# Performance work log

Measured on AMD Instinct MI355X. Metric: run time of the kernel, lower is better.

## Reference

```python
import jax, jax.numpy as jnp
import numpy as np

C_IN = 256


def setup_inputs() -> dict:
    key = jax.random.key(0)
    ks = jax.random.split(key, 10)
    B, C, H, W = 1, C_IN, 96, 96
    Cq = C // 8
    s = 0.05
    return {
        "x": jax.random.normal(ks[0], (B, C, H, W), dtype=jnp.float32),
        "Wq": jax.random.normal(ks[1], (Cq, C), dtype=jnp.float32) * s,
        "bq": jax.random.normal(ks[2], (Cq,), dtype=jnp.float32) * s,
        "Wk": jax.random.normal(ks[3], (Cq, C), dtype=jnp.float32) * s,
        "bk": jax.random.normal(ks[4], (Cq,), dtype=jnp.float32) * s,
        "Wv": jax.random.normal(ks[5], (C, C), dtype=jnp.float32) * s,
        "bv": jax.random.normal(ks[6], (C,), dtype=jnp.float32) * s,
        "W6": jax.random.normal(ks[7], (C, C), dtype=jnp.float32) * s,
        "b6": jax.random.normal(ks[8], (C,), dtype=jnp.float32) * s,
        "gamma": jnp.ones((1,), dtype=jnp.float32),
    }


def reference(x, Wq, bq, Wk, bk, Wv, bv, W6, b6, gamma):
    # TRM forward (OFS just wraps it). 1x1 convs expressed as einsums.
    B, C, H, W = x.shape
    N = H * W
    scale = C ** -0.5  # 1 / sqrt(in_dim)
    xf = x.reshape(B, C, N)
    q = jnp.einsum('oc,bcn->bon', Wq, xf) + bq[None, :, None]   # (B, C/8, N)
    k = jnp.einsum('oc,bcn->bon', Wk, xf) + bk[None, :, None]   # (B, C/8, N)
    v = jnp.einsum('oc,bcn->bon', Wv, xf) + bv[None, :, None]   # (B, C,   N)
    # energy[b,n,m] = sum_c q[b,c,n] * k[b,c,m]  -> full spatial attention (B,N,N)
    energy = jnp.einsum('bcn,bcm->bnm', q, k)
    att = jax.nn.softmax(energy, axis=-1)
    # out[b,c,n] = sum_m v[b,c,m] * att[b,n,m]
    out = jnp.einsum('bcm,bnm->bcn', v, att)                    # (B, C, N)
    # torch: out.permute(2,0,1) -> (N,B,C); max/mean over C; sum; mean over B
    out_co = out.max(axis=1) + out.mean(axis=1)                 # (B, N)
    x_co = out_co.mean(axis=0).reshape(B, -1) * scale           # valid because B == 1
    x_co = jax.nn.softmax(x_co, axis=-1).reshape(B, 1, H, W)    # spatial gate
    gated = x * x_co
    y = jnp.einsum('oc,bchw->bohw', W6, gated) + b6[None, :, None, None]
    return gamma * y + x + y
```

## Files before the change

### kernel.cpp

```cpp
#include <hip/hip_runtime.h>

#define N 9216
#define CIN 256
#define DQ 32
#define NT 144
#define LOG2E 1.44269504088896340736f

typedef short short8 __attribute__((ext_vector_type(8)));
typedef float floatx4 __attribute__((ext_vector_type(4)));
typedef unsigned short ushort_t;

__device__ __forceinline__ ushort_t f2bf(float f) {
  union { float f; unsigned u; } a; a.f = f;
  unsigned u = a.u;
  u += 0x7fffu + ((u >> 16) & 1u);
  return (ushort_t)(u >> 16);
}
__device__ __forceinline__ ushort_t f2bf_fast(float f) {
  union { float f; unsigned u; } a; a.f = f;
  return (ushort_t)((a.u + 0x8000u) >> 16);
}
__device__ __forceinline__ float bf2f(ushort_t h) {
  union { unsigned u; float f; } a; a.u = ((unsigned)h) << 16;
  return a.f;
}
__device__ __forceinline__ unsigned pack2(float lo, float hi) {
  return ((unsigned)f2bf_fast(hi) << 16) | (unsigned)f2bf_fast(lo);
}
__device__ __forceinline__ short8 mk_bf16x8(const float* p) {
  float4 f0 = *(const float4*)(p);
  float4 f1 = *(const float4*)(p + 4);
  union { unsigned u[4]; short8 v; } r;
  r.u[0] = pack2(f0.x, f0.y);
  r.u[1] = pack2(f0.z, f0.w);
  r.u[2] = pack2(f1.x, f1.y);
  r.u[3] = pack2(f1.z, f1.w);
  return r.v;
}

#define XBT_STRIDE 264

__device__ __forceinline__ void stage_x_tile(
    const float* __restrict__ x, int n0, int t, ushort_t (*xbT)[XBT_STRIDE])
{
  const int p = t & 31, ng = t >> 5;
  unsigned* base = (unsigned*)&xbT[0][0] + (size_t)(ng * 8) * 132;
#pragma unroll
  for (int cc = 0; cc < 4; ++cc) {
    const int c = cc * 64 + 2 * p;
    const float* r0 = x + (size_t)c * N + n0 + ng * 8;
    const float* r1 = r0 + N;
    float4 a0 = *(const float4*)(r0);
    float4 a1 = *(const float4*)(r0 + 4);
    float4 b0 = *(const float4*)(r1);
    float4 b1 = *(const float4*)(r1 + 4);
    unsigned* d = base + (cc * 32 + p);
    d[0 * 132] = pack2(a0.x, b0.x);
    d[1 * 132] = pack2(a0.y, b0.y);
    d[2 * 132] = pack2(a0.z, b0.z);
    d[3 * 132] = pack2(a0.w, b0.w);
    d[4 * 132] = pack2(a1.x, b1.x);
    d[5 * 132] = pack2(a1.y, b1.y);
    d[6 * 132] = pack2(a1.z, b1.z);
    d[7 * 132] = pack2(a1.w, b1.w);
  }
}

__global__ __launch_bounds__(256) void qkv_mfma(
    const float* __restrict__ x,
    const float* __restrict__ Wq, const float* __restrict__ bq,
    const float* __restrict__ Wk, const float* __restrict__ bk,
    const float* __restrict__ Wv, const float* __restrict__ bv,
    ushort_t* __restrict__ qT, ushort_t* __restrict__ kT,
    ushort_t* __restrict__ vG, float* __restrict__ sumExp)
{
  if (blockIdx.x == 0 && blockIdx.y == 0 && threadIdx.x == 0) *sumExp = 0.f;

  __shared__ ushort_t xbT[64][XBT_STRIDE];
  const int t = threadIdx.x;
  const int n0 = blockIdx.x * 64;
  const int oc = blockIdx.y;
  const int w = t >> 6, lane = t & 63;
  const int quad = lane >> 4, l15 = lane & 15;

  stage_x_tile(x, n0, t, xbT);
  __syncthreads();

  const int obase = oc * 64 + w * 16;
  const int oA = obase + l15;
  const float* Arow;
  if (oc == 0) Arow = (obase < 32) ? (Wq + (size_t)oA * CIN)
                                   : (Wk + (size_t)(oA - 32) * CIN);
  else         Arow = Wv + (size_t)(oA - 64) * CIN;

  floatx4 acc[4];
#pragma unroll
  for (int b2 = 0; b2 < 4; ++b2) acc[b2] = (floatx4){0.f, 0.f, 0.f, 0.f};

#pragma unroll
  for (int ks = 0; ks < 8; ++ks) {
    const short8 af = mk_bf16x8(Arow + ks * 32 + 8 * quad);
#pragma unroll
    for (int b2 = 0; b2 < 4; ++b2) {
      const short8 bf = *(const short8*)&xbT[b2 * 16 + l15][ks * 32 + 8 * quad];
      acc[b2] = __builtin_amdgcn_mfma_f32_16x16x32_bf16(af, bf, acc[b2], 0, 0, 0);
    }
  }

#pragma unroll
  for (int b2 = 0; b2 < 4; ++b2) {
    const int n = n0 + b2 * 16 + l15;
#pragma unroll
    for (int r = 0; r < 4; ++r) {
      const int o = obase + 4 * quad + r;
      const float val = acc[b2][r];
      if (oc == 0) {
        if (o < 32) qT[(size_t)n * DQ + o]        = f2bf((val + bq[o]) * LOG2E);
        else        kT[(size_t)n * DQ + (o - 32)] = f2bf(val + bk[o - 32]);
      } else        vG[(size_t)(o - 64) * N + n]  = f2bf(val + bv[o - 64]);
    }
  }
}

__global__ __launch_bounds__(256, 4) void attn_kernel(
    const ushort_t* __restrict__ qT, const ushort_t* __restrict__ kT,
    const ushort_t* __restrict__ vG,
    ushort_t* __restrict__ Opart, float* __restrict__ lpart,
    int base, int rem)
{
  __shared__ ushort_t Pb[2][64][36];

  const int t = threadIdx.x;
  const int w = t >> 6;
  const int lane = t & 63;
  const int quad = lane >> 4;
  const int l15 = lane & 15;
  const int nt = blockIdx.x;
  const int s  = blockIdx.y;
  const int n0 = nt * 64;
  const int sliceIters = base + (s < rem ? 1 : 0);
  const int it0 = s * base + (s < rem ? s : rem);
  const int mbase = it0 * 32;
  const int cw = w * 64;

  short8 aq = *(const short8*)(qT + (size_t)(n0 + 16 * w + l15) * DQ + 8 * quad);

  floatx4 acc[4][4];
#pragma unroll
  for (int a2 = 0; a2 < 4; ++a2)
#pragma unroll
    for (int b2 = 0; b2 < 4; ++b2)
      acc[a2][b2] = (floatx4){0.f, 0.f, 0.f, 0.f};
  float lsum[4] = {0.f, 0.f, 0.f, 0.f};
  const floatx4 z4 = {0.f, 0.f, 0.f, 0.f};

  for (int it = 0; it < sliceIters; ++it) {
    const int m0 = mbase + it * 32;

    short8 kb0 = *(const short8*)(kT + (size_t)(m0 + l15) * DQ + 8 * quad);
    short8 kb1 = *(const short8*)(kT + (size_t)(m0 + 16 + l15) * DQ + 8 * quad);
    floatx4 s0 = __builtin_amdgcn_mfma_f32_16x16x32_bf16(aq, kb0, z4, 0, 0, 0);
    floatx4 s1 = __builtin_amdgcn_mfma_f32_16x16x32_bf16(aq, kb1, z4, 0, 0, 0);

    const ushort_t* vb = vG + (size_t)m0 + 8 * quad;
    short8 av0 = *(const short8*)(vb + (size_t)(cw +  0 + l15) * N);
    short8 av1 = *(const short8*)(vb + (size_t)(cw + 16 + l15) * N);
    short8 av2 = *(const short8*)(vb + (size_t)(cw + 32 + l15) * N);
    short8 av3 = *(const short8*)(vb + (size_t)(cw + 48 + l15) * N);

    ushort_t* pb = &Pb[it & 1][0][0];
#pragma unroll
    for (int r = 0; r < 4; ++r) {
      float p0 = exp2f(s0[r]);
      float p1 = exp2f(s1[r]);
      lsum[r] += p0 + p1;
      const int row = 16 * w + 4 * quad + r;
      pb[row * 36 + l15]      = f2bf_fast(p0);
      pb[row * 36 + 16 + l15] = f2bf_fast(p1);
    }
    __syncthreads();

#pragma unroll
    for (int b2 = 0; b2 < 4; ++b2) {
      const ushort_t* pr = pb + (b2 * 16 + l15) * 36 + 8 * quad;
      union { uint2 u2[2]; short8 v; } u;
      u.u2[0] = *(const uint2*)(pr);
      u.u2[1] = *(const uint2*)(pr + 4);
      const short8 pf = u.v;
      acc[0][b2] = __builtin_amdgcn_mfma_f32_16x16x32_bf16(av0, pf, acc[0][b2], 0, 0, 0);
      acc[1][b2] = __builtin_amdgcn_mfma_f32_16x16x32_bf16(av1, pf, acc[1][b2], 0, 0, 0);
      acc[2][b2] = __builtin_amdgcn_mfma_f32_16x16x32_bf16(av2, pf, acc[2][b2], 0, 0, 0);
      acc[3][b2] = __builtin_amdgcn_mfma_f32_16x16x32_bf16(av3, pf, acc[3][b2], 0, 0, 0);
    }
  }

#pragma unroll
  for (int r = 0; r < 4; ++r) {
    float v = lsum[r];
    v += __shfl_xor(v, 1);
    v += __shfl_xor(v, 2);
    v += __shfl_xor(v, 4);
    v += __shfl_xor(v, 8);
    lsum[r] = v;
  }
  if (l15 == 0) {
#pragma unroll
    for (int r = 0; r < 4; ++r)
      lpart[(size_t)s * N + n0 + 16 * w + 4 * quad + r] = lsum[r];
  }

  const size_t basep = ((size_t)s * NT + nt) * 256;
#pragma unroll
  for (int a2 = 0; a2 < 4; ++a2)
#pragma unroll
    for (int b2 = 0; b2 < 4; ++b2)
#pragma unroll
      for (int r = 0; r < 4; ++r) {
        const int c  = cw + a2 * 16 + 4 * quad + r;
        const int nl = b2 * 16 + l15;
        Opart[(basep + c) * 64 + nl] = f2bf(acc[a2][b2][r]);
      }
}

template<int NSL>
__global__ __launch_bounds__(1024) void cco_kernel(
    const ushort_t* __restrict__ Opart, const float* __restrict__ lpart,
    float* __restrict__ e_buf, float* __restrict__ sumExp)
{
  const int nt = blockIdx.x;
  const int t = threadIdx.x;
  const int n = t & 63, ci = t >> 6;
  float mx = -3.4e38f, sm = 0.f;
#pragma unroll
  for (int k = 0; k < 16; ++k) {
    const int c = ci * 16 + k;
    float val = 0.f;
#pragma unroll
    for (int s2 = 0; s2 < NSL; ++s2)
      val += bf2f(Opart[(((size_t)s2 * NT + nt) * 256 + c) * 64 + n]);
    mx = fmaxf(mx, val);
    sm += val;
  }
  __shared__ float rmx[16][64], rsm[16][64];
  rmx[ci][n] = mx; rsm[ci][n] = sm;
  __syncthreads();
  if (t < 64) {
    float m = rmx[0][t], s = rsm[0][t];
#pragma unroll
    for (int g = 1; g < 16; ++g) { m = fmaxf(m, rmx[g][t]); s += rsm[g][t]; }
    float l = 0.f;
#pragma unroll
    for (int s3 = 0; s3 < NSL; ++s3) l += lpart[(size_t)s3 * N + nt * 64 + t];
    const float oc = (m + s * (1.0f / 256.0f)) / l;
    const float ev = exp2f(oc * (0.0625f * LOG2E));
    e_buf[nt * 64 + t] = ev;
    float vs = ev;
    vs += __shfl_xor(vs, 1);  vs += __shfl_xor(vs, 2);
    vs += __shfl_xor(vs, 4);  vs += __shfl_xor(vs, 8);
    vs += __shfl_xor(vs, 16); vs += __shfl_xor(vs, 32);
    if (t == 0) atomicAdd(sumExp, vs);
  }
}

__global__ __launch_bounds__(256) void final_mfma(
    const float* __restrict__ x, const float* __restrict__ W6,
    const float* __restrict__ b6, const float* __restrict__ gamma,
    const float* __restrict__ e_buf, const float* __restrict__ sumExp,
    float* __restrict__ out)
{
  __shared__ ushort_t xbT[64][XBT_STRIDE];
  const int t = threadIdx.x;
  const int n0 = blockIdx.x * 64;
  const int w = t >> 6, lane = t & 63;
  const int quad = lane >> 4, l15 = lane & 15;

  stage_x_tile(x, n0, t, xbT);
  __syncthreads();

  const int obase = blockIdx.y * 64 + w * 16;
  const float* Arow = W6 + (size_t)(obase + l15) * CIN;

  floatx4 acc[4];
#pragma unroll
  for (int b2 = 0; b2 < 4; ++b2) acc[b2] = (floatx4){0.f, 0.f, 0.f, 0.f};

#pragma unroll
  for (int ks = 0; ks < 8; ++ks) {
    const short8 af = mk_bf16x8(Arow + ks * 32 + 8 * quad);
#pragma unroll
    for (int b2 = 0; b2 < 4; ++b2) {
      const short8 bf = *(const short8*)&xbT[b2 * 16 + l15][ks * 32 + 8 * quad];
      acc[b2] = __builtin_amdgcn_mfma_f32_16x16x32_bf16(af, bf, acc[b2], 0, 0, 0);
    }
  }

  const float g1 = 1.0f + gamma[0];
  const float inv = 1.0f / sumExp[0];
#pragma unroll
  for (int b2 = 0; b2 < 4; ++b2) {
    const int n = n0 + b2 * 16 + l15;
    const float xc = e_buf[n] * inv;
#pragma unroll
    for (int r = 0; r < 4; ++r) {
      const int o = obase + 4 * quad + r;
      const float xv = x[(size_t)o * N + n];
      out[(size_t)o * N + n] = xv + g1 * (xc * acc[b2][r] + b6[o]);
    }
  }
}

extern "C" void kernel_launch(void* const* d_in, const int* in_sizes, int n_in,
                              void* d_out, int out_size, void* d_ws, size_t ws_size,
                              hipStream_t stream)
{
  const float* x     = (const float*)d_in[0];
  const float* Wq    = (const float*)d_in[1];
  const float* bq    = (const float*)d_in[2];
  const float* Wk    = (const float*)d_in[3];
  const float* bk    = (const float*)d_in[4];
  const float* Wv    = (const float*)d_in[5];
  const float* bv    = (const float*)d_in[6];
  const float* W6    = (const float*)d_in[7];
  const float* b6    = (const float*)d_in[8];
  const float* gamma = (const float*)d_in[9];
  float* out = (float*)d_out;

  const size_t fixed = (size_t)N * DQ * 2 * 2
                     + (size_t)CIN * N * 2
                     + (size_t)N * 4
                     + 256;
  int nsl = 7;
  size_t need = fixed + (size_t)nsl * NT * 256 * 64 * 2 + (size_t)nsl * N * 4;
  if (ws_size < need) nsl = 4;
  const int totIters = N / 32;
  const int base = totIters / nsl;
  const int rem  = totIters % nsl;

  char* ws = (char*)d_ws;
  const size_t OFF_QT = 0;
  const size_t OFF_KT = OFF_QT + (size_t)N * DQ * 2;
  const size_t OFF_V  = OFF_KT + (size_t)N * DQ * 2;
  const size_t OFF_OP = OFF_V  + (size_t)CIN * N * 2;
  const size_t OFF_LP = OFF_OP + (size_t)nsl * NT * 256 * 64 * 2;
  const size_t OFF_EB = OFF_LP + (size_t)nsl * N * 4;
  const size_t OFF_SE = OFF_EB + (size_t)N * 4;

  ushort_t* qT     = (ushort_t*)(ws + OFF_QT);
  ushort_t* kT     = (ushort_t*)(ws + OFF_KT);
  ushort_t* vG     = (ushort_t*)(ws + OFF_V);
  ushort_t* Opart  = (ushort_t*)(ws + OFF_OP);
  float*    lpart  = (float*)(ws + OFF_LP);
  float*    e_buf  = (float*)(ws + OFF_EB);
  float*    sumExp = (float*)(ws + OFF_SE);

  qkv_mfma<<<dim3(NT, 5), 256, 0, stream>>>(x, Wq, bq, Wk, bk, Wv, bv, qT, kT, vG, sumExp);
  attn_kernel<<<dim3(NT, nsl), 256, 0, stream>>>(qT, kT, vG, Opart, lpart, base, rem);
  if (nsl == 7) cco_kernel<7><<<NT, 1024, 0, stream>>>(Opart, lpart, e_buf, sumExp);
  else          cco_kernel<4><<<NT, 1024, 0, stream>>>(Opart, lpart, e_buf, sumExp);
  final_mfma<<<dim3(NT, 4), 256, 0, stream>>>(x, W6, b6, gamma, e_buf, sumExp, out);
}
```

Baseline: 216.0 us.

## Split attention work across 8 waves per block to cut per-wave registers

New measurement: 230.8 us. 1.07x slower.

```diff
diff --git a/kernel.cpp b/kernel.cpp
--- a/kernel.cpp
+++ b/kernel.cpp
@@ -122,64 +122,66 @@
   }
 }
 
-__global__ __launch_bounds__(256, 4) void attn_kernel(
+__global__ __launch_bounds__(512, 6) void attn_kernel(
     const ushort_t* __restrict__ qT, const ushort_t* __restrict__ kT,
     const ushort_t* __restrict__ vG,
     ushort_t* __restrict__ Opart, float* __restrict__ lpart,
     int base, int rem)
 {
   __shared__ ushort_t Pb[2][64][36];
+  __shared__ float lred[2][64];
 
   const int t = threadIdx.x;
   const int w = t >> 6;
   const int lane = t & 63;
   const int quad = lane >> 4;
   const int l15 = lane & 15;
+  const int nq = w & 3;
+  const int mq = w >> 2;
   const int nt = blockIdx.x;
   const int s  = blockIdx.y;
   const int n0 = nt * 64;
   const int sliceIters = base + (s < rem ? 1 : 0);
   const int it0 = s * base + (s < rem ? s : rem);
   const int mbase = it0 * 32;
-  const int cw = w * 64;
-
-  short8 aq = *(const short8*)(qT + (size_t)(n0 + 16 * w + l15) * DQ + 8 * quad);
-
-  floatx4 acc[4][4];
-#pragma unroll
-  for (int a2 = 0; a2 < 4; ++a2)
+  const int cw = w * 32;
+
+  const short8 aq =
+      *(const short8*)(qT + (size_t)(n0 + 16 * nq + l15) * DQ + 8 * quad);
+
+  floatx4 acc[2][4];
+#pragma unroll
+  for (int a2 = 0; a2 < 2; ++a2)
 #pragma unroll
     for (int b2 = 0; b2 < 4; ++b2)
       acc[a2][b2] = (floatx4){0.f, 0.f, 0.f, 0.f};
   float lsum[4] = {0.f, 0.f, 0.f, 0.f};
   const floatx4 z4 = {0.f, 0.f, 0.f, 0.f};
 
+  const ushort_t* kPtr =
+      kT + (size_t)(mbase + 16 * mq + l15) * DQ + 8 * quad;
+  const ushort_t* vPtr =
+      vG + (size_t)(cw + l15) * N + mbase + 8 * quad;
+
   for (int it = 0; it < sliceIters; ++it) {
-    const int m0 = mbase + it * 32;
-
-    short8 kb0 = *(const short8*)(kT + (size_t)(m0 + l15) * DQ + 8 * quad);
-    short8 kb1 = *(const short8*)(kT + (size_t)(m0 + 16 + l15) * DQ + 8 * quad);
-    floatx4 s0 = __builtin_amdgcn_mfma_f32_16x16x32_bf16(aq, kb0, z4, 0, 0, 0);
-    floatx4 s1 = __builtin_amdgcn_mfma_f32_16x16x32_bf16(aq, kb1, z4, 0, 0, 0);
-
-    const ushort_t* vb = vG + (size_t)m0 + 8 * quad;
-    short8 av0 = *(const short8*)(vb + (size_t)(cw +  0 + l15) * N);
-    short8 av1 = *(const short8*)(vb + (size_t)(cw + 16 + l15) * N);
-    short8 av2 = *(const short8*)(vb + (size_t)(cw + 32 + l15) * N);
-    short8 av3 = *(const short8*)(vb + (size_t)(cw + 48 + l15) * N);
+    const short8 kb = *(const short8*)(kPtr);
+    kPtr += 32 * DQ;
+    floatx4 sv = __builtin_amdgcn_mfma_f32_16x16x32_bf16(aq, kb, z4, 0, 0, 0);
+
+    const short8 av0 = *(const short8*)(vPtr);
+    const short8 av1 = *(const short8*)(vPtr + (size_t)16 * N);
+    vPtr += 32;
 
     ushort_t* pb = &Pb[it & 1][0][0];
 #pragma unroll
     for (int r = 0; r < 4; ++r) {
-      float p0 = exp2f(s0[r]);
-      float p1 = exp2f(s1[r]);
-      lsum[r] += p0 + p1;
-      const int row = 16 * w + 4 * quad + r;
-      pb[row * 36 + l15]      = f2bf_fast(p0);
-      pb[row * 36 + 16 + l15] = f2bf_fast(p1);
+      float p = exp2f(sv[r]);
+      lsum[r] += p;
+      pb[(16 * nq + 4 * quad + r) * 36 + 16 * mq + l15] = f2bf_fast(p);
     }
     __syncthreads();
 
+    __builtin_amdgcn_s_setprio(1);
 #pragma unroll
     for (int b2 = 0; b2 < 4; ++b2) {
       const ushort_t* pr = pb + (b2 * 16 + l15) * 36 + 8 * quad;
@@ -189,9 +191,8 @@
       const short8 pf = u.v;
       acc[0][b2] = __builtin_amdgcn_mfma_f32_16x16x32_bf16(av0, pf, acc[0][b2], 0, 0, 0);
       acc[1][b2] = __builtin_amdgcn_mfma_f32_16x16x32_bf16(av1, pf, acc[1][b2], 0, 0, 0);
-      acc[2][b2] = __builtin_amdgcn_mfma_f32_16x16x32_bf16(av2, pf, acc[2][b2], 0, 0, 0);
-      acc[3][b2] = __builtin_amdgcn_mfma_f32_16x16x32_bf16(av3, pf, acc[3][b2], 0, 0, 0);
-    }
+    }
+    __builtin_amdgcn_s_setprio(0);
   }
 
 #pragma unroll
@@ -206,12 +207,15 @@
   if (l15 == 0) {
 #pragma unroll
     for (int r = 0; r < 4; ++r)
-      lpart[(size_t)s * N + n0 + 16 * w + 4 * quad + r] = lsum[r];
-  }
+      lred[mq][16 * nq + 4 * quad + r] = lsum[r];
+  }
+  __syncthreads();
+  if (t < 64)
+    lpart[(size_t)s * N + n0 + t] = lred[0][t] + lred[1][t];
 
   const size_t basep = ((size_t)s * NT + nt) * 256;
 #pragma unroll
-  for (int a2 = 0; a2 < 4; ++a2)
+  for (int a2 = 0; a2 < 2; ++a2)
 #pragma unroll
     for (int b2 = 0; b2 < 4; ++b2)
 #pragma unroll
@@ -354,7 +358,7 @@
   float*    sumExp = (float*)(ws + OFF_SE);
 
   qkv_mfma<<<dim3(NT, 5), 256, 0, stream>>>(x, Wq, bq, Wk, bk, Wv, bv, qT, kT, vG, sumExp);
-  attn_kernel<<<dim3(NT, nsl), 256, 0, stream>>>(qT, kT, vG, Opart, lpart, base, rem);
+  attn_kernel<<<dim3(NT, nsl), 512, 0, stream>>>(qT, kT, vG, Opart, lpart, base, rem);
   if (nsl == 7) cco_kernel<7><<<NT, 1024, 0, stream>>>(Opart, lpart, e_buf, sumExp);
   else          cco_kernel<4><<<NT, 1024, 0, stream>>>(Opart, lpart, e_buf, sumExp);
   final_mfma<<<dim3(NT, 4), 256, 0, stream>>>(x, W6, b6, gamma, e_buf, sumExp, out);
```

## Software-pipeline attention loop: prefetch K/V, overlap next QK softmax with PV MMA

Applied to the files above, without the earlier changes.

Result: no change. 214.2 us (-0.8%).

```diff
diff --git a/kernel.cpp b/kernel.cpp
--- a/kernel.cpp
+++ b/kernel.cpp
@@ -122,7 +122,7 @@
   }
 }
 
-__global__ __launch_bounds__(256, 4) void attn_kernel(
+__global__ __launch_bounds__(256, 3) void attn_kernel(
     const ushort_t* __restrict__ qT, const ushort_t* __restrict__ kT,
     const ushort_t* __restrict__ vG,
     ushort_t* __restrict__ Opart, float* __restrict__ lpart,
@@ -143,7 +143,8 @@
   const int mbase = it0 * 32;
   const int cw = w * 64;
 
-  short8 aq = *(const short8*)(qT + (size_t)(n0 + 16 * w + l15) * DQ + 8 * quad);
+  const short8 aq =
+      *(const short8*)(qT + (size_t)(n0 + 16 * w + l15) * DQ + 8 * quad);
 
   floatx4 acc[4][4];
 #pragma unroll
@@ -154,21 +155,30 @@
   float lsum[4] = {0.f, 0.f, 0.f, 0.f};
   const floatx4 z4 = {0.f, 0.f, 0.f, 0.f};
 
-  for (int it = 0; it < sliceIters; ++it) {
-    const int m0 = mbase + it * 32;
-
-    short8 kb0 = *(const short8*)(kT + (size_t)(m0 + l15) * DQ + 8 * quad);
-    short8 kb1 = *(const short8*)(kT + (size_t)(m0 + 16 + l15) * DQ + 8 * quad);
-    floatx4 s0 = __builtin_amdgcn_mfma_f32_16x16x32_bf16(aq, kb0, z4, 0, 0, 0);
-    floatx4 s1 = __builtin_amdgcn_mfma_f32_16x16x32_bf16(aq, kb1, z4, 0, 0, 0);
-
-    const ushort_t* vb = vG + (size_t)m0 + 8 * quad;
-    short8 av0 = *(const short8*)(vb + (size_t)(cw +  0 + l15) * N);
-    short8 av1 = *(const short8*)(vb + (size_t)(cw + 16 + l15) * N);
-    short8 av2 = *(const short8*)(vb + (size_t)(cw + 32 + l15) * N);
-    short8 av3 = *(const short8*)(vb + (size_t)(cw + 48 + l15) * N);
-
-    ushort_t* pb = &Pb[it & 1][0][0];
+  const ushort_t* kRow  = kT + (size_t)(mbase + l15) * DQ + 8 * quad;
+  const ushort_t* vRow0 = vG + (size_t)(cw +  0 + l15) * N + mbase + 8 * quad;
+  const ushort_t* vRow1 = vG + (size_t)(cw + 16 + l15) * N + mbase + 8 * quad;
+  const ushort_t* vRow2 = vG + (size_t)(cw + 32 + l15) * N + mbase + 8 * quad;
+  const ushort_t* vRow3 = vG + (size_t)(cw + 48 + l15) * N + mbase + 8 * quad;
+
+  short8 k0 = *(const short8*)(kRow);
+  short8 k1 = *(const short8*)(kRow + 16 * DQ);
+  kRow += 32 * DQ;
+  floatx4 s0 = __builtin_amdgcn_mfma_f32_16x16x32_bf16(aq, k0, z4, 0, 0, 0);
+  floatx4 s1 = __builtin_amdgcn_mfma_f32_16x16x32_bf16(aq, k1, z4, 0, 0, 0);
+
+  short8 avU0 = *(const short8*)(vRow0);
+  short8 avU1 = *(const short8*)(vRow1);
+  short8 avU2 = *(const short8*)(vRow2);
+  short8 avU3 = *(const short8*)(vRow3);
+  vRow0 += 32; vRow1 += 32; vRow2 += 32; vRow3 += 32;
+
+  short8 kbU0 = *(const short8*)(kRow);
+  short8 kbU1 = *(const short8*)(kRow + 16 * DQ);
+  kRow += 32 * DQ;
+
+  {
+    ushort_t* pb = &Pb[0][0][0];
 #pragma unroll
     for (int r = 0; r < 4; ++r) {
       float p0 = exp2f(s0[r]);
@@ -178,20 +188,91 @@
       pb[row * 36 + l15]      = f2bf_fast(p0);
       pb[row * 36 + 16 + l15] = f2bf_fast(p1);
     }
+  }
+  __syncthreads();
+
+  for (int it = 0; it < sliceIters - 1; ++it) {
+    const ushort_t* pbR = &Pb[it & 1][0][0];
+    ushort_t*       pbW = &Pb[(it + 1) & 1][0][0];
+
+    union { uint2 u2[2]; short8 v; } pu0, pu1, pu2, pu3;
+    {
+      const ushort_t* pr0 = pbR + (0 * 16 + l15) * 36 + 8 * quad;
+      const ushort_t* pr1 = pbR + (1 * 16 + l15) * 36 + 8 * quad;
+      const ushort_t* pr2 = pbR + (2 * 16 + l15) * 36 + 8 * quad;
+      const ushort_t* pr3 = pbR + (3 * 16 + l15) * 36 + 8 * quad;
+      pu0.u2[0] = *(const uint2*)(pr0); pu0.u2[1] = *(const uint2*)(pr0 + 4);
+      pu1.u2[0] = *(const uint2*)(pr1); pu1.u2[1] = *(const uint2*)(pr1 + 4);
+      pu2.u2[0] = *(const uint2*)(pr2); pu2.u2[1] = *(const uint2*)(pr2 + 4);
+      pu3.u2[0] = *(const uint2*)(pr3); pu3.u2[1] = *(const uint2*)(pr3 + 4);
+    }
+
+    short8 kbV0 = *(const short8*)(kRow);
+    short8 kbV1 = *(const short8*)(kRow + 16 * DQ);
+    kRow += 32 * DQ;
+    short8 avV0 = *(const short8*)(vRow0);
+    short8 avV1 = *(const short8*)(vRow1);
+    short8 avV2 = *(const short8*)(vRow2);
+    short8 avV3 = *(const short8*)(vRow3);
+    vRow0 += 32; vRow1 += 32; vRow2 += 32; vRow3 += 32;
+
+    floatx4 t0 = __builtin_amdgcn_mfma_f32_16x16x32_bf16(aq, kbU0, z4, 0, 0, 0);
+    floatx4 t1 = __builtin_amdgcn_mfma_f32_16x16x32_bf16(aq, kbU1, z4, 0, 0, 0);
+
+#pragma unroll
+    for (int r = 0; r < 4; ++r) {
+      float p0 = exp2f(t0[r]);
+      float p1 = exp2f(t1[r]);
+      lsum[r] += p0 + p1;
+      const int row = 16 * w + 4 * quad + r;
+      pbW[row * 36 + l15]      = f2bf_fast(p0);
+      pbW[row * 36 + 16 + l15] = f2bf_fast(p1);
+    }
+
+    __builtin_amdgcn_s_setprio(1);
+    {
+      const short8 pf0 = pu0.v, pf1 = pu1.v, pf2 = pu2.v, pf3 = pu3.v;
+      acc[0][0] = __builtin_amdgcn_mfma_f32_16x16x32_bf16(avU0, pf0, acc[0][0], 0, 0, 0);
+      acc[1][0] = __builtin_amdgcn_mfma_f32_16x16x32_bf16(avU1, pf0, acc[1][0], 0, 0, 0);
+      acc[2][0] = __builtin_amdgcn_mfma_f32_16x16x32_bf16(avU2, pf0, acc[2][0], 0, 0, 0);
+      acc[3][0] = __builtin_amdgcn_mfma_f32_16x16x32_bf16(avU3, pf0, acc[3][0], 0, 0, 0);
+      acc[0][1] = __builtin_amdgcn_mfma_f32_16x16x32_bf16(avU0, pf1, acc[0][1], 0, 0, 0);
+      acc[1][1] = __builtin_amdgcn_mfma_f32_16x16x32_bf16(avU1, pf1, acc[1][1], 0, 0, 0);
+      acc[2][1] = __builtin_amdgcn_mfma_f32_16x16x32_bf16(avU2, pf1, acc[2][1], 0, 0, 0);
+      acc[3][1] = __builtin_amdgcn_mfma_f32_16x16x32_bf16(avU3, pf1, acc[3][1], 0, 0, 0);
+      acc[0][2] = __builtin_amdgcn_mfma_f32_16x16x32_bf16(avU0, pf2, acc[0][2], 0, 0, 0);
+      acc[1][2] = __builtin_amdgcn_mfma_f32_16x16x32_bf16(avU1, pf2, acc[1][2], 0, 0, 0);
+      acc[2][2] = __builtin_amdgcn_mfma_f32_16x16x32_bf16(avU2, pf2, acc[2][2], 0, 0, 0);
+      acc[3][2] = __builtin_amdgcn_mfma_f32_16x16x32_bf16(avU3, pf2, acc[3][2], 0, 0, 0);
+      acc[0][3] = __builtin_amdgcn_mfma_f32_16x16x32_bf16(avU0, pf3, acc[0][3], 0, 0, 0);
+      acc[1][3] = __builtin_amdgcn_mfma_f32_16x16x32_bf16(avU1, pf3, acc[1][3], 0, 0, 0);
+      acc[2][3] = __builtin_amdgcn_mfma_f32_16x16x32_bf16(avU2, pf3, acc[2][3], 0, 0, 0);
+      acc[3][3] = __builtin_amdgcn_mfma_f32_16x16x32_bf16(avU3, pf3, acc[3][3], 0, 0, 0);
+    }
+    __builtin_amdgcn_s_setprio(0);
+
+    kbU0 = kbV0; kbU1 = kbV1;
+    avU0 = avV0; avU1 = avV1; avU2 = avV2; avU3 = avV3;
+
     __syncthreads();
-
+  }
+
+  {
+    const ushort_t* pbR = &Pb[(sliceIters - 1) & 1][0][0];
+    __builtin_amdgcn_s_setprio(1);
 #pragma unroll
     for (int b2 = 0; b2 < 4; ++b2) {
-      const ushort_t* pr = pb + (b2 * 16 + l15) * 36 + 8 * quad;
+      const ushort_t* pr = pbR + (b2 * 16 + l15) * 36 + 8 * quad;
       union { uint2 u2[2]; short8 v; } u;
       u.u2[0] = *(const uint2*)(pr);
       u.u2[1] = *(const uint2*)(pr + 4);
       const short8 pf = u.v;
-      acc[0][b2] = __builtin_amdgcn_mfma_f32_16x16x32_bf16(av0, pf, acc[0][b2], 0, 0, 0);
-      acc[1][b2] = __builtin_amdgcn_mfma_f32_16x16x32_bf16(av1, pf, acc[1][b2], 0, 0, 0);
-      acc[2][b2] = __builtin_amdgcn_mfma_f32_16x16x32_bf16(av2, pf, acc[2][b2], 0, 0, 0);
-      acc[3][b2] = __builtin_amdgcn_mfma_f32_16x16x32_bf16(av3, pf, acc[3][b2], 0, 0, 0);
-    }
+      acc[0][b2] = __builtin_amdgcn_mfma_f32_16x16x32_bf16(avU0, pf, acc[0][b2], 0, 0, 0);
+      acc[1][b2] = __builtin_amdgcn_mfma_f32_16x16x32_bf16(avU1, pf, acc[1][b2], 0, 0, 0);
+      acc[2][b2] = __builtin_amdgcn_mfma_f32_16x16x32_bf16(avU2, pf, acc[2][b2], 0, 0, 0);
+      acc[3][b2] = __builtin_amdgcn_mfma_f32_16x16x32_bf16(avU3, pf, acc[3][b2], 0, 0, 0);
+    }
+    __builtin_amdgcn_s_setprio(0);
   }
 
 #pragma unroll
```

## Split attention into single-wave blocks per channel slice, dropping block barriers

Applied to the files above, without the earlier changes.

Result: slower. 231.5 us (+7.2%).

```diff
diff --git a/kernel.cpp b/kernel.cpp
--- a/kernel.cpp
+++ b/kernel.cpp
@@ -122,28 +122,30 @@
   }
 }
 
-__global__ __launch_bounds__(256, 4) void attn_kernel(
+__global__ __launch_bounds__(64, 2) void attn_kernel(
     const ushort_t* __restrict__ qT, const ushort_t* __restrict__ kT,
     const ushort_t* __restrict__ vG,
     ushort_t* __restrict__ Opart, float* __restrict__ lpart,
     int base, int rem)
 {
-  __shared__ ushort_t Pb[2][64][36];
+  __shared__ ushort_t Pl[64][40];
 
   const int t = threadIdx.x;
-  const int w = t >> 6;
-  const int lane = t & 63;
-  const int quad = lane >> 4;
-  const int l15 = lane & 15;
+  const int quad = t >> 4;
+  const int l15 = t & 15;
   const int nt = blockIdx.x;
   const int s  = blockIdx.y;
+  const int cs = blockIdx.z;
   const int n0 = nt * 64;
+  const int cw = cs * 64;
   const int sliceIters = base + (s < rem ? 1 : 0);
   const int it0 = s * base + (s < rem ? s : rem);
   const int mbase = it0 * 32;
-  const int cw = w * 64;
-
-  short8 aq = *(const short8*)(qT + (size_t)(n0 + 16 * w + l15) * DQ + 8 * quad);
+
+  short8 aq[4];
+#pragma unroll
+  for (int b2 = 0; b2 < 4; ++b2)
+    aq[b2] = *(const short8*)(qT + (size_t)(n0 + b2 * 16 + l15) * DQ + 8 * quad);
 
   floatx4 acc[4][4];
 #pragma unroll
@@ -154,59 +156,74 @@
   float lsum[4] = {0.f, 0.f, 0.f, 0.f};
   const floatx4 z4 = {0.f, 0.f, 0.f, 0.f};
 
+  const ushort_t* kRow = kT + (size_t)(mbase + l15) * DQ + 8 * quad;
+  const ushort_t* vRow = vG + (size_t)(cw + l15) * N + mbase + 8 * quad;
+
+  short8 kbU0 = *(const short8*)(kRow);
+  short8 kbU1 = *(const short8*)(kRow + 16 * DQ);
+  kRow += 32 * DQ;
+
   for (int it = 0; it < sliceIters; ++it) {
-    const int m0 = mbase + it * 32;
-
-    short8 kb0 = *(const short8*)(kT + (size_t)(m0 + l15) * DQ + 8 * quad);
-    short8 kb1 = *(const short8*)(kT + (size_t)(m0 + 16 + l15) * DQ + 8 * quad);
-    floatx4 s0 = __builtin_amdgcn_mfma_f32_16x16x32_bf16(aq, kb0, z4, 0, 0, 0);
-    floatx4 s1 = __builtin_amdgcn_mfma_f32_16x16x32_bf16(aq, kb1, z4, 0, 0, 0);
-
-    const ushort_t* vb = vG + (size_t)m0 + 8 * quad;
-    short8 av0 = *(const short8*)(vb + (size_t)(cw +  0 + l15) * N);
-    short8 av1 = *(const short8*)(vb + (size_t)(cw + 16 + l15) * N);
-    short8 av2 = *(const short8*)(vb + (size_t)(cw + 32 + l15) * N);
-    short8 av3 = *(const short8*)(vb + (size_t)(cw + 48 + l15) * N);
-
-    ushort_t* pb = &Pb[it & 1][0][0];
-#pragma unroll
-    for (int r = 0; r < 4; ++r) {
-      float p0 = exp2f(s0[r]);
-      float p1 = exp2f(s1[r]);
-      lsum[r] += p0 + p1;
-      const int row = 16 * w + 4 * quad + r;
-      pb[row * 36 + l15]      = f2bf_fast(p0);
-      pb[row * 36 + 16 + l15] = f2bf_fast(p1);
-    }
-    __syncthreads();
-
-#pragma unroll
-    for (int b2 = 0; b2 < 4; ++b2) {
-      const ushort_t* pr = pb + (b2 * 16 + l15) * 36 + 8 * quad;
-      union { uint2 u2[2]; short8 v; } u;
-      u.u2[0] = *(const uint2*)(pr);
-      u.u2[1] = *(const uint2*)(pr + 4);
-      const short8 pf = u.v;
+    const short8 av0 = *(const short8*)(vRow);
+    const short8 av1 = *(const short8*)(vRow + (size_t)16 * N);
+    const short8 av2 = *(const short8*)(vRow + (size_t)32 * N);
+    const short8 av3 = *(const short8*)(vRow + (size_t)48 * N);
+    vRow += 32;
+    const short8 kbV0 = *(const short8*)(kRow);
+    const short8 kbV1 = *(const short8*)(kRow + 16 * DQ);
+    kRow += 32 * DQ;
+
+    floatx4 slo[4], shi[4];
+#pragma unroll
+    for (int b2 = 0; b2 < 4; ++b2) {
+      slo[b2] = __builtin_amdgcn_mfma_f32_16x16x32_bf16(kbU0, aq[b2], z4, 0, 0, 0);
+      shi[b2] = __builtin_amdgcn_mfma_f32_16x16x32_bf16(kbU1, aq[b2], z4, 0, 0, 0);
+    }
+
+#pragma unroll
+    for (int b2 = 0; b2 < 4; ++b2) {
+      const float pl0 = exp2f(slo[b2][0]);
+      const float pl1 = exp2f(slo[b2][1]);
+      const float pl2 = exp2f(slo[b2][2]);
+      const float pl3 = exp2f(slo[b2][3]);
+      const float ph0 = exp2f(shi[b2][0]);
+      const float ph1 = exp2f(shi[b2][1]);
+      const float ph2 = exp2f(shi[b2][2]);
+      const float ph3 = exp2f(shi[b2][3]);
+      lsum[b2] += ((pl0 + pl1) + (pl2 + pl3)) + ((ph0 + ph1) + (ph2 + ph3));
+      uint2 lo, hi;
+      lo.x = pack2(pl0, pl1); lo.y = pack2(pl2, pl3);
+      hi.x = pack2(ph0, ph1); hi.y = pack2(ph2, ph3);
+      const int n = b2 * 16 + l15;
+      *(uint2*)&Pl[n][4 * quad]      = lo;
+      *(uint2*)&Pl[n][16 + 4 * quad] = hi;
+    }
+
+    __builtin_amdgcn_s_setprio(1);
+#pragma unroll
+    for (int b2 = 0; b2 < 4; ++b2) {
+      const short8 pf = *(const short8*)&Pl[b2 * 16 + l15][8 * quad];
       acc[0][b2] = __builtin_amdgcn_mfma_f32_16x16x32_bf16(av0, pf, acc[0][b2], 0, 0, 0);
       acc[1][b2] = __builtin_amdgcn_mfma_f32_16x16x32_bf16(av1, pf, acc[1][b2], 0, 0, 0);
       acc[2][b2] = __builtin_amdgcn_mfma_f32_16x16x32_bf16(av2, pf, acc[2][b2], 0, 0, 0);
       acc[3][b2] = __builtin_amdgcn_mfma_f32_16x16x32_bf16(av3, pf, acc[3][b2], 0, 0, 0);
     }
-  }
-
-#pragma unroll
-  for (int r = 0; r < 4; ++r) {
-    float v = lsum[r];
-    v += __shfl_xor(v, 1);
-    v += __shfl_xor(v, 2);
-    v += __shfl_xor(v, 4);
-    v += __shfl_xor(v, 8);
-    lsum[r] = v;
-  }
-  if (l15 == 0) {
-#pragma unroll
-    for (int r = 0; r < 4; ++r)
-      lpart[(size_t)s * N + n0 + 16 * w + 4 * quad + r] = lsum[r];
+    __builtin_amdgcn_s_setprio(0);
+
+    kbU0 = kbV0; kbU1 = kbV1;
+  }
+
+#pragma unroll
+  for (int b2 = 0; b2 < 4; ++b2) {
+    float v = lsum[b2];
+    v += __shfl_xor(v, 16);
+    v += __shfl_xor(v, 32);
+    lsum[b2] = v;
+  }
+  if (cs == 0 && t < 16) {
+#pragma unroll
+    for (int b2 = 0; b2 < 4; ++b2)
+      lpart[(size_t)s * N + n0 + b2 * 16 + t] = lsum[b2];
   }
 
   const size_t basep = ((size_t)s * NT + nt) * 256;
@@ -354,7 +371,7 @@
   float*    sumExp = (float*)(ws + OFF_SE);
 
   qkv_mfma<<<dim3(NT, 5), 256, 0, stream>>>(x, Wq, bq, Wk, bk, Wv, bv, qT, kT, vG, sumExp);
-  attn_kernel<<<dim3(NT, nsl), 256, 0, stream>>>(qT, kT, vG, Opart, lpart, base, rem);
+  attn_kernel<<<dim3(NT, nsl, 4), 64, 0, stream>>>(qT, kT, vG, Opart, lpart, base, rem);
   if (nsl == 7) cco_kernel<7><<<NT, 1024, 0, stream>>>(Opart, lpart, e_buf, sumExp);
   else          cco_kernel<4><<<NT, 1024, 0, stream>>>(Opart, lpart, e_buf, sumExp);
   final_mfma<<<dim3(NT, 4), 256, 0, stream>>>(x, W6, b6, gamma, e_buf, sumExp, out);
```
